# Performance work log

Measured on AMD Instinct MI355X. Metric: run time of the kernel, lower is better.

The kernel has to match this reference:

```python
import jax, jax.numpy as jnp
import numpy as np

DIM = 768
H = 12          # num_heads
KV = 4          # kv_heads
D = DIM // H    # head_dim = 64
ROPE_BASE = 10000.0
WINDOW = 8
B, N = 4, 1024


def setup_inputs() -> dict:
    key = jax.random.key(0)
    ks = jax.random.split(key, 8)
    s = 0.02  # weight scale for sane magnitudes
    return {
        "x": jax.random.normal(ks[0], (B, N, DIM), jnp.float32),
        "Wq": jax.random.normal(ks[1], (2 * DIM, DIM), jnp.float32) * s,
        "Wk": jax.random.normal(ks[2], (2 * DIM * KV // H, DIM), jnp.float32) * s,
        "Wv1": jax.random.normal(ks[3], (DIM * KV // H, DIM), jnp.float32) * s,
        "Wv2": jax.random.normal(ks[4], (DIM * KV // H, DIM), jnp.float32) * s,
        "lambda_p": jnp.full((H, 1, 1), -2.0, jnp.float32),
        "Wo": jax.random.normal(ks[5], (DIM, DIM), jnp.float32) * s,
        "bo": jax.random.normal(ks[6], (DIM,), jnp.float32) * s,
    }


def _rotate_half(x):
    x1 = x[..., ::2]
    x2 = x[..., 1::2]
    return jnp.stack([-x2, x1], axis=-1).reshape(x.shape)


def _rope_cos_sin(n, dtype):
    side = int(n ** 0.5)
    if side * side == n:
        h = np.arange(side, dtype=np.float32)
        gh, gw = np.meshgrid(h, h, indexing="ij")
        pos_h, pos_w = gh.reshape(-1), gw.reshape(-1)
    else:
        pos_h = np.arange(n, dtype=np.float32)
        pos_w = np.zeros_like(pos_h)
    dim_half = D // 2
    inv_freq = ROPE_BASE ** (-np.arange(dim_half, dtype=np.float32) / dim_half)
    theta = np.concatenate([pos_h[:, None] * inv_freq[None, :],
                            pos_w[:, None] * inv_freq[None, :]], axis=1)  # [N, D]
    cos = jnp.asarray(np.cos(theta), dtype)[None, None]  # [1,1,N,D]
    sin = jnp.asarray(np.sin(theta), dtype)[None, None]
    return cos, sin


def _apply_rope(q, cos, sin):
    return q * cos + _rotate_half(q) * sin


def _qk_norm(t):
    return t / (jnp.linalg.norm(t, axis=-1, keepdims=True) + 1e-6)


def _window_mask(n, dtype):
    side = int(n ** 0.5)
    if side * side == n:
        h = np.arange(side)
        gh, gw = np.meshgrid(h, h, indexing="ij")
        coords = np.stack([gh.reshape(-1), gw.reshape(-1)], axis=1)  # [N,2]
        dist = np.abs(coords[:, None, :] - coords[None, :, :]).max(-1)  # Chebyshev
    else:
        idx = np.arange(n)
        dist = np.abs(idx[None, :] - idx[:, None])
    return jnp.asarray(np.where(dist > WINDOW, -np.inf, 0.0).astype(np.float32), dtype)


def _attend(q, k, v, mask):
    # q,k,v: [B,H,N,D]; mask additive [N,N]
    scale = 1.0 / np.sqrt(D)
    scores = jnp.einsum("bhnd,bhmd->bhnm", q, k) * scale + mask
    return jnp.einsum("bhnm,bhmd->bhnd", jax.nn.softmax(scores, axis=-1), v)


def reference(x, Wq, Wk, Wv1, Wv2, lambda_p, Wo, bo):
    b, n, c = x.shape
    rep = H // KV
    q = (x @ Wq.T).reshape(b, n, 2, H, D).transpose(2, 0, 3, 1, 4)   # [2,B,H,N,D]
    k = (x @ Wk.T).reshape(b, n, 2, KV, D).transpose(2, 0, 3, 1, 4)  # [2,B,KV,N,D]
    v1 = (x @ Wv1.T).reshape(b, n, KV, D).transpose(0, 2, 1, 3)      # [B,KV,N,D]
    v2 = (x @ Wv2.T).reshape(b, n, KV, D).transpose(0, 2, 1, 3)
    q1, q2 = q[0], q[1]
    k1, k2 = k[0], k[1]
    # GQA: repeat_interleave over head axis
    k1 = jnp.repeat(k1, rep, axis=1)
    k2 = jnp.repeat(k2, rep, axis=1)
    v1 = jnp.repeat(v1, rep, axis=1)
    v2 = jnp.repeat(v2, rep, axis=1)
    cos, sin = _rope_cos_sin(n, x.dtype)
    q1, q2 = _apply_rope(q1, cos, sin), _apply_rope(q2, cos, sin)
    k1, k2 = _apply_rope(k1, cos, sin), _apply_rope(k2, cos, sin)
    q1, q2, k1, k2 = _qk_norm(q1), _qk_norm(q2), _qk_norm(k1), _qk_norm(k2)
    mask = _window_mask(n, x.dtype)
    out1 = _attend(q1, k1, v1, mask)
    out2 = _attend(q2, k2, v2, mask)
    lam = jax.nn.softplus(lambda_p)  # [H,1,1] broadcasts over [B,H,N,D]
    out = out1 - lam[None] * out2
    out = out.transpose(0, 2, 1, 3).reshape(b, n, c)
    return out @ Wo.T + bo
```

## Files before the change

kernel.cpp:

```cpp
#include <hip/hip_runtime.h>
#include <hip/hip_bf16.h>

#define BATCH 4
#define NSEQ  1024
#define DIM   768
#define NH    12
#define NKV   4
#define HD    64
#define NTOK  (BATCH*NSEQ)

using bf16 = __hip_bfloat16;
typedef __attribute__((ext_vector_type(8))) short short8;
typedef __attribute__((ext_vector_type(4))) float floatx4;

__device__ __forceinline__ float b2f(short x) {
  unsigned u = ((unsigned)(unsigned short)x) << 16;
  return __builtin_bit_cast(float, u);
}
__device__ __forceinline__ unsigned short f2b(float f) {
  unsigned u = __builtin_bit_cast(unsigned, f);
  unsigned r = u + 0x7FFF + ((u >> 16) & 1);
  return (unsigned short)(r >> 16);
}
__device__ __forceinline__ unsigned cvtpk(float lo, float hi) {
  unsigned r;
  asm("v_cvt_pk_bf16_f32 %0, %1, %2" : "=v"(r) : "v"(lo), "v"(hi));
  return r;
}

__device__ __forceinline__ void load_lds_16(const bf16* g, bf16* l) {
  __builtin_amdgcn_global_load_lds(
      (const __attribute__((address_space(1))) void*)g,
      (__attribute__((address_space(3))) void*)l, 16, 0, 0);
}

__global__ __launch_bounds__(256) void cvt_all(
    const float* __restrict__ x,  const float* __restrict__ wq,
    const float* __restrict__ wk, const float* __restrict__ wv1,
    const float* __restrict__ wv2, const float* __restrict__ wo,
    bf16* __restrict__ xb,  bf16* __restrict__ wqb, bf16* __restrict__ wkb,
    bf16* __restrict__ wv1b, bf16* __restrict__ wv2b, bf16* __restrict__ wob)
{
  int i = blockIdx.x * 256 + threadIdx.x;
  const float* s; bf16* d; int off;
  if      (i <  786432) { s = x;   d = xb;   off = i; }
  else if (i < 1081344) { s = wq;  d = wqb;  off = i -  786432; }
  else if (i < 1179648) { s = wk;  d = wkb;  off = i - 1081344; }
  else if (i < 1228800) { s = wv1; d = wv1b; off = i - 1179648; }
  else if (i < 1277952) { s = wv2; d = wv2b; off = i - 1228800; }
  else                  { s = wo;  d = wob;  off = i - 1277952; }
  float4 f = reinterpret_cast<const float4*>(s)[off];
  ushort4 u;
  u.x = f2b(f.x); u.y = f2b(f.y); u.z = f2b(f.z); u.w = f2b(f.w);
  reinterpret_cast<ushort4*>(d)[off] = u;
}

__global__ __launch_bounds__(256, 2) void gemm_qkv(
    const bf16* __restrict__ xb,
    const bf16* __restrict__ Wqb, const bf16* __restrict__ Wkb,
    const bf16* __restrict__ Wv1b, const bf16* __restrict__ Wv2b,
    bf16* __restrict__ Qpk, bf16* __restrict__ Kpk,
    bf16* __restrict__ Vpk1, bf16* __restrict__ Vpk2)
{
  __shared__ __align__(16) bf16 As[128 * 64];
  __shared__ __align__(16) bf16 Ws[128 * 64];

  const int bn = blockIdx.x, bm = blockIdx.y;
  const bf16* Wp;
  if (bn < 12)      Wp = Wqb  + (size_t)bn * 128 * 768;
  else if (bn < 16) Wp = Wkb  + (size_t)(bn - 12) * 128 * 768;
  else if (bn < 18) Wp = Wv1b + (size_t)(bn - 16) * 128 * 768;
  else              Wp = Wv2b + (size_t)(bn - 18) * 128 * 768;

  const int t = threadIdx.x, wave = t >> 6, lane = t & 63;
  const int wm = wave >> 1, wn = wave & 1;
  const int quad = lane >> 4, lr = lane & 15;

  const int srow = wave * 32 + (lane >> 3);
  const int scol = ((lane & 7) ^ (lane >> 3)) * 8;
  const bf16* Ag = xb + (size_t)(bm * 128 + srow) * 768 + scol;
  const bf16* Wg = Wp + (size_t)srow * 768 + scol;
  bf16* Al = As + wave * 32 * 64;
  bf16* Wl = Ws + wave * 32 * 64;

  floatx4 acc[4][4] = {};

  for (int k0 = 0; k0 < 768; k0 += 64) {
    #pragma unroll
    for (int c = 0; c < 4; ++c) {
      load_lds_16(Ag + (size_t)c * 8 * 768 + k0, Al + c * 8 * 64);
      load_lds_16(Wg + (size_t)c * 8 * 768 + k0, Wl + c * 8 * 64);
    }
    __syncthreads();

    short8 af[4][2], wf[4][2];
    #pragma unroll
    for (int mt = 0; mt < 4; ++mt)
      #pragma unroll
      for (int ks = 0; ks < 2; ++ks)
        af[mt][ks] = *reinterpret_cast<const short8*>(
            &As[(wm * 64 + mt * 16 + lr) * 64 + ((ks * 32 + quad * 8) ^ ((lr & 7) * 8))]);
    #pragma unroll
    for (int nt = 0; nt < 4; ++nt)
      #pragma unroll
      for (int ks = 0; ks < 2; ++ks)
        wf[nt][ks] = *reinterpret_cast<const short8*>(
            &Ws[(wn * 64 + nt * 16 + lr) * 64 + ((ks * 32 + quad * 8) ^ ((lr & 7) * 8))]);

    #pragma unroll
    for (int mt = 0; mt < 4; ++mt)
      #pragma unroll
      for (int nt = 0; nt < 4; ++nt) {
        acc[mt][nt] = __builtin_amdgcn_mfma_f32_16x16x32_bf16(af[mt][0], wf[nt][0], acc[mt][nt], 0, 0, 0);
        acc[mt][nt] = __builtin_amdgcn_mfma_f32_16x16x32_bf16(af[mt][1], wf[nt][1], acc[mt][nt], 0, 0, 0);
      }
    __syncthreads();
  }

  if (bn < 16) {
    const float K2 = 0.41524101186098309f;
    const float invf0 = exp2f(-(float)lr * K2);
    const float invf1 = exp2f(-(float)(16 + lr) * K2);
    const float sgn = (lr & 1) ? 1.f : -1.f;
    const bool isq = (bn < 12);
    const int hq = bn * 2 + wn;
    const int sq_ = hq / 12, hq_ = hq % 12;
    const int hh = (bn - 12) * 2 + wn;
    const int sk_ = hh >> 2, kvh_ = hh & 3;
    const int qk128 = (lr >> 3) * 128;
    #pragma unroll
    for (int mt = 0; mt < 4; ++mt) {
      const int row0 = bm * 128 + wm * 64 + mt * 16 + quad * 4;
      const int n0 = row0 & (NSEQ - 1);
      const int bb = row0 >> 10, kh = n0 >> 5;
      const float ph = (float)kh;
      const float pw0 = (float)(n0 & 31);
      const float t0 = ph * invf0, t1 = ph * invf1;
      const float c0 = __cosf(t0), s0 = __sinf(t0);
      const float c1 = __cosf(t1), s1 = __sinf(t1);
      bf16* tb0;
      if (isq) {
        tb0 = Qpk + ((size_t)((bb * 2 + sq_) * 12 + hq_) * 32 + kh) * 2048
              + (size_t)(mt & 1) * 1024 + qk128 + (quad * 4) * 8 + (lr & 7);
      } else {
        tb0 = Kpk + ((size_t)((bb * 2 + sk_) * 4 + kvh_) * 32 + kh) * 2048
              + (size_t)(mt & 1) * 1024 + qk128 + (quad * 4) * 8 + (lr & 7);
      }
      #pragma unroll
      for (int r = 0; r < 4; ++r) {
        float v0 = acc[mt][0][r];
        float v1 = acc[mt][1][r];
        float v2 = acc[mt][2][r];
        float v3 = acc[mt][3][r];
        float rot0 = sgn * __shfl_xor(v0, 1);
        float rot1 = sgn * __shfl_xor(v1, 1);
        float rot2 = sgn * __shfl_xor(v2, 1);
        float rot3 = sgn * __shfl_xor(v3, 1);
        float pw = pw0 + (float)r;
        float t2 = pw * invf0, t3 = pw * invf1;
        float rv0 = v0 * c0 + rot0 * s0;
        float rv1 = v1 * c1 + rot1 * s1;
        float rv2 = v2 * __cosf(t2) + rot2 * __sinf(t2);
        float rv3 = v3 * __cosf(t3) + rot3 * __sinf(t3);
        float ss = rv0 * rv0 + rv1 * rv1 + rv2 * rv2 + rv3 * rv3;
        #pragma unroll
        for (int off = 1; off < 16; off <<= 1) ss += __shfl_xor(ss, off);
        float sc = 1.f / (sqrtf(ss) + 1e-6f);
        if (isq) sc *= 0.18033688011112042f;
        bf16* tb = tb0 + r * 8;
        unsigned pkA = cvtpk(rv0 * sc, rv1 * sc);
        unsigned pkB = cvtpk(rv2 * sc, rv3 * sc);
        *(unsigned short*)&tb[0]   = (unsigned short)pkA;
        *(unsigned short*)&tb[256] = (unsigned short)(pkA >> 16);
        *(unsigned short*)&tb[512] = (unsigned short)pkB;
        *(unsigned short*)&tb[768] = (unsigned short)(pkB >> 16);
      }
    }
  } else {
    const bool is2 = (bn >= 18);
    bf16* Vp = is2 ? Vpk2 : Vpk1;
    const int kvh_ = (bn - (is2 ? 18 : 16)) * 2 + wn;
    #pragma unroll
    for (int mt = 0; mt < 4; ++mt)
      #pragma unroll
      for (int r = 0; r < 4; ++r) {
        int row = bm * 128 + wm * 64 + mt * 16 + quad * 4 + r;
        int n = row & (NSEQ - 1);
        int bb = row >> 10, kh = n >> 5;
        int rowm = (mt & 1) * 16 + quad * 4 + r;
        int quad_v = rowm >> 3, j = rowm & 7;
        bf16* tb = Vp + ((size_t)(bb * 4 + kvh_) * 32 + kh) * 2048
                   + quad_v * 128 + lr * 8 + j;
        unsigned pkA = cvtpk(acc[mt][0][r], acc[mt][1][r]);
        unsigned pkB = cvtpk(acc[mt][2][r], acc[mt][3][r]);
        *(unsigned short*)&tb[0]    = (unsigned short)pkA;
        *(unsigned short*)&tb[512]  = (unsigned short)(pkA >> 16);
        *(unsigned short*)&tb[1024] = (unsigned short)pkB;
        *(unsigned short*)&tb[1536] = (unsigned short)(pkB >> 16);
      }
  }
}

__global__ __launch_bounds__(256) void gemm_out(
    const bf16* __restrict__ Xb, const bf16* __restrict__ Wob,
    float* __restrict__ out, const float* __restrict__ bias)
{
  __shared__ __align__(16) bf16 As[64 * 64];
  __shared__ __align__(16) bf16 Ws[64 * 64];

  const int bn = blockIdx.x, bm = blockIdx.y;
  const int t = threadIdx.x, wave = t >> 6, lane = t & 63;
  const int wm = wave >> 1, wn = wave & 1;
  const int quad = lane >> 4, lr = lane & 15;

  const int srow = wave * 16 + (lane >> 3);
  const int scol = ((lane & 7) ^ (lane >> 3)) * 8;
  const bf16* Ag = Xb  + (size_t)(bm * 64 + srow) * 768 + scol;
  const bf16* Wg = Wob + (size_t)(bn * 64 + srow) * 768 + scol;
  bf16* Al = As + wave * 16 * 64;
  bf16* Wl = Ws + wave * 16 * 64;

  floatx4 acc[2][2] = {};

  for (int k0 = 0; k0 < 768; k0 += 64) {
    #pragma unroll
    for (int c = 0; c < 2; ++c) {
      load_lds_16(Ag + (size_t)c * 8 * 768 + k0, Al + c * 8 * 64);
      load_lds_16(Wg + (size_t)c * 8 * 768 + k0, Wl + c * 8 * 64);
    }
    __syncthreads();

    short8 af[2][2], wf[2][2];
    #pragma unroll
    for (int mt = 0; mt < 2; ++mt)
      #pragma unroll
      for (int ks = 0; ks < 2; ++ks)
        af[mt][ks] = *reinterpret_cast<const short8*>(
            &As[(wm * 32 + mt * 16 + lr) * 64 + ((ks * 32 + quad * 8) ^ ((lr & 7) * 8))]);
    #pragma unroll
    for (int nt = 0; nt < 2; ++nt)
      #pragma unroll
      for (int ks = 0; ks < 2; ++ks)
        wf[nt][ks] = *reinterpret_cast<const short8*>(
            &Ws[(wn * 32 + nt * 16 + lr) * 64 + ((ks * 32 + quad * 8) ^ ((lr & 7) * 8))]);

    #pragma unroll
    for (int mt = 0; mt < 2; ++mt)
      #pragma unroll
      for (int nt = 0; nt < 2; ++nt) {
        acc[mt][nt] = __builtin_amdgcn_mfma_f32_16x16x32_bf16(af[mt][0], wf[nt][0], acc[mt][nt], 0, 0, 0);
        acc[mt][nt] = __builtin_amdgcn_mfma_f32_16x16x32_bf16(af[mt][1], wf[nt][1], acc[mt][nt], 0, 0, 0);
      }
    __syncthreads();
  }

  #pragma unroll
  for (int nt = 0; nt < 2; ++nt) {
    int col = bn * 64 + wn * 32 + nt * 16 + lr;
    float bv = bias[col];
    #pragma unroll
    for (int mt = 0; mt < 2; ++mt)
      #pragma unroll
      for (int r = 0; r < 4; ++r) {
        int row = bm * 64 + wm * 32 + mt * 16 + quad * 4 + r;
        out[(size_t)row * 768 + col] = acc[mt][nt][r] + bv;
      }
  }
}

struct Frag { short8 kf[2][2]; short8 vf[4]; };

__device__ __forceinline__ void attn_load(
    Frag& f, const bf16* __restrict__ kp, const bf16* __restrict__ vp,
    int kh, int lane8)
{
  const bf16* kt = kp + (size_t)kh * 2048 + lane8;
  const bf16* vt = vp + (size_t)kh * 2048 + lane8;
  f.kf[0][0] = *reinterpret_cast<const short8*>(kt);
  f.kf[0][1] = *reinterpret_cast<const short8*>(kt + 512);
  f.kf[1][0] = *reinterpret_cast<const short8*>(kt + 1024);
  f.kf[1][1] = *reinterpret_cast<const short8*>(kt + 1536);
  f.vf[0] = *reinterpret_cast<const short8*>(vt);
  f.vf[1] = *reinterpret_cast<const short8*>(vt + 512);
  f.vf[2] = *reinterpret_cast<const short8*>(vt + 1024);
  f.vf[3] = *reinterpret_cast<const short8*>(vt + 1536);
}

__device__ __forceinline__ void attn_step(
    const short8 (&qf)[2][2], const Frag& f, unsigned maskbits,
    floatx4 (&O)[2][4], float (&psum)[2][4], bf16* __restrict__ Pl,
    int quad, int lr)
{
  floatx4 S[2][2] = {};
  #pragma unroll
  for (int ks = 0; ks < 2; ++ks) {
    S[0][0] = __builtin_amdgcn_mfma_f32_16x16x32_bf16(qf[0][ks], f.kf[0][ks], S[0][0], 0, 0, 0);
    S[0][1] = __builtin_amdgcn_mfma_f32_16x16x32_bf16(qf[0][ks], f.kf[1][ks], S[0][1], 0, 0, 0);
    S[1][0] = __builtin_amdgcn_mfma_f32_16x16x32_bf16(qf[1][ks], f.kf[0][ks], S[1][0], 0, 0, 0);
    S[1][1] = __builtin_amdgcn_mfma_f32_16x16x32_bf16(qf[1][ks], f.kf[1][ks], S[1][1], 0, 0, 0);
  }

  #pragma unroll
  for (int mt = 0; mt < 2; ++mt)
    #pragma unroll
    for (int nt = 0; nt < 2; ++nt) {
      float pr[4];
      #pragma unroll
      for (int r = 0; r < 4; ++r) {
        float p = __builtin_amdgcn_exp2f(S[mt][nt][r]);
        p = ((maskbits >> (mt * 8 + nt * 4 + r)) & 1u) ? p : 0.0f;
        psum[mt][r] += p;
        pr[r] = p;
      }
      unsigned pkA = cvtpk(pr[0], pr[1]);
      unsigned pkB = cvtpk(pr[2], pr[3]);
      unsigned short* bp = (unsigned short*)&Pl[(mt * 16 + quad * 4) * 40 + nt * 16 + lr];
      bp[0]   = (unsigned short)pkA;
      bp[40]  = (unsigned short)(pkA >> 16);
      bp[80]  = (unsigned short)pkB;
      bp[120] = (unsigned short)(pkB >> 16);
    }

  short8 pf0 = *reinterpret_cast<const short8*>(&Pl[(lr) * 40 + quad * 8]);
  short8 pf1 = *reinterpret_cast<const short8*>(&Pl[(16 + lr) * 40 + quad * 8]);
  #pragma unroll
  for (int ntd = 0; ntd < 4; ++ntd) {
    O[0][ntd] = __builtin_amdgcn_mfma_f32_16x16x32_bf16(pf0, f.vf[ntd], O[0][ntd], 0, 0, 0);
    O[1][ntd] = __builtin_amdgcn_mfma_f32_16x16x32_bf16(pf1, f.vf[ntd], O[1][ntd], 0, 0, 0);
  }
}

__global__ __launch_bounds__(256, 2) void attn_mfma(
    const bf16* __restrict__ Qpk, const bf16* __restrict__ Kpk,
    const bf16* __restrict__ Vpk1, const bf16* __restrict__ Vpk2,
    const float* __restrict__ lambda_p, bf16* __restrict__ X)
{
  __shared__ __align__(16) char smem[20480];

  const int bid = blockIdx.x;
  const int qh = bid & 31;
  const int hb = bid >> 5;
  const int h  = hb % 12;
  const int b  = hb / 12;
  const int kvh = h / 3;

  const int t = threadIdx.x;
  const int w = t >> 6;
  const int s = w >> 1;
  const int half = w & 1;
  const int lane = t & 63;
  const int quad = lane >> 4, lr = lane & 15;
  const int lane8 = lane * 8;

  bf16* Pl = (bf16*)(smem + w * 2560);
  float* myO = (float*)(smem + (s ? 10240 : 0));
  float* myP = (float*)(smem + (s ? 10240 : 0) + 8192);
  bf16* Xs = (bf16*)smem;

  const int tok0 = b * NSEQ + qh * 32;

  short8 qf[2][2];
  {
    const bf16* qt = Qpk + ((size_t)((b * 2 + s) * 12 + h) * 32 + qh) * 2048 + lane8;
    qf[0][0] = *reinterpret_cast<const short8*>(qt);
    qf[0][1] = *reinterpret_cast<const short8*>(qt + 512);
    qf[1][0] = *reinterpret_cast<const short8*>(qt + 1024);
    qf[1][1] = *reinterpret_cast<const short8*>(qt + 1536);
  }

  unsigned maskbits = 0;
  #pragma unroll
  for (int mt = 0; mt < 2; ++mt)
    #pragma unroll
    for (int nt = 0; nt < 2; ++nt)
      #pragma unroll
      for (int r = 0; r < 4; ++r) {
        int qq = mt * 16 + quad * 4 + r;
        int km = nt * 16 + lr;
        int d = km - qq; if (d < 0) d = -d;
        if (d <= 8) maskbits |= 1u << (mt * 8 + nt * 4 + r);
      }

  floatx4 O[2][4] = {};
  float psum[2][4] = {};

  const int kh0 = (qh > 8) ? qh - 8 : 0;
  const int kh1 = (qh < 23) ? qh + 8 : 31;
  const int cnt = kh1 - kh0 + 1;
  const int cA = (cnt + 1) >> 1;
  const int khA = half ? kh0 + cA : kh0;
  const int khB = half ? kh1 : kh0 + cA - 1;

  const bf16* kpbase = Kpk + (size_t)((b * 2 + s) * 4 + kvh) * 32 * 2048;
  const bf16* vpbase = (s ? Vpk2 : Vpk1) + (size_t)(b * 4 + kvh) * 32 * 2048;

  Frag fA, fB;
  attn_load(fA, kpbase, vpbase, khA, lane8);
  attn_load(fB, kpbase, vpbase, (khA + 1 <= khB) ? khA + 1 : khB, lane8);

  int i = khA;
  while (true) {
    attn_step(qf, fA, maskbits, O, psum, Pl, quad, lr);
    if (i == khB) break;
    ++i;
    attn_load(fA, kpbase, vpbase, (i + 1 <= khB) ? i + 1 : i, lane8);
    attn_step(qf, fB, maskbits, O, psum, Pl, quad, lr);
    if (i == khB) break;
    ++i;
    attn_load(fB, kpbase, vpbase, (i + 1 <= khB) ? i + 1 : i, lane8);
  }

  auto writeslab = [&]() {
    #pragma unroll
    for (int mt = 0; mt < 2; ++mt)
      #pragma unroll
      for (int ntd = 0; ntd < 4; ++ntd)
        *reinterpret_cast<floatx4*>(&myO[(mt * 4 + ntd) * 256 + lane * 4]) = O[mt][ntd];
    floatx4 p0, p1;
    p0[0] = psum[0][0]; p0[1] = psum[0][1]; p0[2] = psum[0][2]; p0[3] = psum[0][3];
    p1[0] = psum[1][0]; p1[1] = psum[1][1]; p1[2] = psum[1][2]; p1[3] = psum[1][3];
    *reinterpret_cast<floatx4*>(&myP[lane * 4])       = p0;
    *reinterpret_cast<floatx4*>(&myP[256 + lane * 4]) = p1;
  };
  auto readadd_norm = [&]() {
    #pragma unroll
    for (int mt = 0; mt < 2; ++mt)
      #pragma unroll
      for (int ntd = 0; ntd < 4; ++ntd)
        O[mt][ntd] += *reinterpret_cast<const floatx4*>(&myO[(mt * 4 + ntd) * 256 + lane * 4]);
    floatx4 p0 = *reinterpret_cast<const floatx4*>(&myP[lane * 4]);
    floatx4 p1 = *reinterpret_cast<const floatx4*>(&myP[256 + lane * 4]);
    #pragma unroll
    for (int r = 0; r < 4; ++r) { psum[0][r] += p0[r]; psum[1][r] += p1[r]; }
    #pragma unroll
    for (int off = 1; off < 16; off <<= 1)
      #pragma unroll
      for (int mt = 0; mt < 2; ++mt)
        #pragma unroll
        for (int r = 0; r < 4; ++r)
          psum[mt][r] += __shfl_xor(psum[mt][r], off);
    #pragma unroll
    for (int mt = 0; mt < 2; ++mt)
      #pragma unroll
      for (int r = 0; r < 4; ++r)
        psum[mt][r] = 1.f / psum[mt][r];
    #pragma unroll
    for (int mt = 0; mt < 2; ++mt)
      #pragma unroll
      for (int ntd = 0; ntd < 4; ++ntd)
        #pragma unroll
        for (int r = 0; r < 4; ++r)
          O[mt][ntd][r] *= psum[mt][r];
  };

  __syncthreads();
  if (half) writeslab();
  __syncthreads();
  if (!half) {
    readadd_norm();
    if (s) {
      #pragma unroll
      for (int mt = 0; mt < 2; ++mt)
        #pragma unroll
        for (int ntd = 0; ntd < 4; ++ntd)
          *reinterpret_cast<floatx4*>(&myO[(mt * 4 + ntd) * 256 + lane * 4]) = O[mt][ntd];
    }
  }
  __syncthreads();
  if (w == 0) {
    const float* O2s = (const float*)(smem + 10240);
    float lam = log1pf(__expf(lambda_p[h]));
    #pragma unroll
    for (int mt = 0; mt < 2; ++mt)
      #pragma unroll
      for (int ntd = 0; ntd < 4; ++ntd) {
        floatx4 o2 = *reinterpret_cast<const floatx4*>(&O2s[(mt * 4 + ntd) * 256 + lane * 4]);
        #pragma unroll
        for (int r = 0; r < 4; ++r) {
          float xv = O[mt][ntd][r] - lam * o2[r];
          *(unsigned short*)&Xs[(mt * 16 + quad * 4 + r) * 72 + ntd * 16 + lr] = f2b(xv);
        }
      }
  }
  __syncthreads();

  {
    int row = t >> 3, seg = t & 7;
    short8 xv = *reinterpret_cast<const short8*>(&Xs[row * 72 + seg * 8]);
    *reinterpret_cast<short8*>(X + (size_t)(tok0 + row) * 768 + h * 64 + seg * 8) = xv;
  }
}

extern "C" void kernel_launch(void* const* d_in, const int* in_sizes, int n_in,
                              void* d_out, int out_size, void* d_ws, size_t ws_size,
                              hipStream_t stream)
{
  const float* x        = (const float*)d_in[0];
  const float* Wq       = (const float*)d_in[1];
  const float* Wk       = (const float*)d_in[2];
  const float* Wv1      = (const float*)d_in[3];
  const float* Wv2      = (const float*)d_in[4];
  const float* lambda_p = (const float*)d_in[5];
  const float* Wo       = (const float*)d_in[6];
  const float* bo       = (const float*)d_in[7];
  float* out = (float*)d_out;

  bf16* xb   = (bf16*)d_ws;
  bf16* Wqb  = xb   + (size_t)NTOK * 768;
  bf16* Wkb  = Wqb  + (size_t)1536 * 768;
  bf16* Wv1b = Wkb  + (size_t)512 * 768;
  bf16* Wv2b = Wv1b + (size_t)256 * 768;
  bf16* Wob  = Wv2b + (size_t)256 * 768;
  bf16* Qpk  = Wob  + (size_t)768 * 768;
  bf16* Xb   = Qpk  + (size_t)NTOK * 1536;
  bf16* Vpk1 = Xb   + (size_t)NTOK * 768;
  bf16* Vpk2 = Vpk1 + (size_t)512 * 2048;
  bf16* Kpk  = Vpk2 + (size_t)512 * 2048;

  cvt_all<<<5568, 256, 0, stream>>>(x, Wq, Wk, Wv1, Wv2, Wo,
                                    xb, Wqb, Wkb, Wv1b, Wv2b, Wob);

  gemm_qkv<<<dim3(20, 32), 256, 0, stream>>>(xb, Wqb, Wkb, Wv1b, Wv2b,
                                             Qpk, Kpk, Vpk1, Vpk2);

  attn_mfma<<<BATCH * NH * 32, 256, 0, stream>>>(Qpk, Kpk, Vpk1, Vpk2, lambda_p, Xb);

  gemm_out<<<dim3(12, 64), 256, 0, stream>>>(Xb, Wob, out, bo);
}
```

Baseline: 146.5 us.

## Compute transposed scores and build P fragments via permlane swaps instead of LDS

Computes S transposed (K as the A operand) so each lane holds probabilities for a single query column. The P operand for the PV MFMA is then assembled in registers with v_permlane32_swap and shuffles, removing the per-step LDS round trip for P. Row sums become one scalar per query with a cheaper reduction, and the normalisation broadcasts the inverse through shuffles. The intent is to cut LDS traffic and waits in the inner loop, at the cost of extra cross-lane operations.

```diff
diff --git a/kernel.cpp b/kernel.cpp
--- a/kernel.cpp
+++ b/kernel.cpp
@@ -12,6 +12,7 @@
 using bf16 = __hip_bfloat16;
 typedef __attribute__((ext_vector_type(8))) short short8;
 typedef __attribute__((ext_vector_type(4))) float floatx4;
+typedef __attribute__((ext_vector_type(4))) unsigned uint4v;
 
 __device__ __forceinline__ float b2f(short x) {
   unsigned u = ((unsigned)(unsigned short)x) << 16;
@@ -288,45 +289,51 @@
 
 __device__ __forceinline__ void attn_step(
     const short8 (&qf)[2][2], const Frag& f, unsigned maskbits,
-    floatx4 (&O)[2][4], float (&psum)[2][4], bf16* __restrict__ Pl,
-    int quad, int lr)
-{
-  floatx4 S[2][2] = {};
+    floatx4 (&O)[2][4], float (&psum)[2], int quad)
+{
+  floatx4 St[2][2] = {};
   #pragma unroll
   for (int ks = 0; ks < 2; ++ks) {
-    S[0][0] = __builtin_amdgcn_mfma_f32_16x16x32_bf16(qf[0][ks], f.kf[0][ks], S[0][0], 0, 0, 0);
-    S[0][1] = __builtin_amdgcn_mfma_f32_16x16x32_bf16(qf[0][ks], f.kf[1][ks], S[0][1], 0, 0, 0);
-    S[1][0] = __builtin_amdgcn_mfma_f32_16x16x32_bf16(qf[1][ks], f.kf[0][ks], S[1][0], 0, 0, 0);
-    S[1][1] = __builtin_amdgcn_mfma_f32_16x16x32_bf16(qf[1][ks], f.kf[1][ks], S[1][1], 0, 0, 0);
-  }
-
+    St[0][0] = __builtin_amdgcn_mfma_f32_16x16x32_bf16(f.kf[0][ks], qf[0][ks], St[0][0], 0, 0, 0);
+    St[0][1] = __builtin_amdgcn_mfma_f32_16x16x32_bf16(f.kf[0][ks], qf[1][ks], St[0][1], 0, 0, 0);
+    St[1][0] = __builtin_amdgcn_mfma_f32_16x16x32_bf16(f.kf[1][ks], qf[0][ks], St[1][0], 0, 0, 0);
+    St[1][1] = __builtin_amdgcn_mfma_f32_16x16x32_bf16(f.kf[1][ks], qf[1][ks], St[1][1], 0, 0, 0);
+  }
+
+  unsigned pk[2][2][2];
   #pragma unroll
-  for (int mt = 0; mt < 2; ++mt)
-    #pragma unroll
-    for (int nt = 0; nt < 2; ++nt) {
+  for (int kt = 0; kt < 2; ++kt)
+    #pragma unroll
+    for (int mt = 0; mt < 2; ++mt) {
       float pr[4];
       #pragma unroll
       for (int r = 0; r < 4; ++r) {
-        float p = __builtin_amdgcn_exp2f(S[mt][nt][r]);
-        p = ((maskbits >> (mt * 8 + nt * 4 + r)) & 1u) ? p : 0.0f;
-        psum[mt][r] += p;
+        float p = __builtin_amdgcn_exp2f(St[kt][mt][r]);
+        p = ((maskbits >> (kt * 8 + mt * 4 + r)) & 1u) ? p : 0.0f;
+        psum[mt] += p;
         pr[r] = p;
       }
-      unsigned pkA = cvtpk(pr[0], pr[1]);
-      unsigned pkB = cvtpk(pr[2], pr[3]);
-      unsigned short* bp = (unsigned short*)&Pl[(mt * 16 + quad * 4) * 40 + nt * 16 + lr];
-      bp[0]   = (unsigned short)pkA;
-      bp[40]  = (unsigned short)(pkA >> 16);
-      bp[80]  = (unsigned short)pkB;
-      bp[120] = (unsigned short)(pkB >> 16);
-    }
-
-  short8 pf0 = *reinterpret_cast<const short8*>(&Pl[(lr) * 40 + quad * 8]);
-  short8 pf1 = *reinterpret_cast<const short8*>(&Pl[(16 + lr) * 40 + quad * 8]);
+      pk[kt][mt][0] = cvtpk(pr[0], pr[1]);
+      pk[kt][mt][1] = cvtpk(pr[2], pr[3]);
+    }
+
+  const bool oddq = (quad & 1);
   #pragma unroll
-  for (int ntd = 0; ntd < 4; ++ntd) {
-    O[0][ntd] = __builtin_amdgcn_mfma_f32_16x16x32_bf16(pf0, f.vf[ntd], O[0][ntd], 0, 0, 0);
-    O[1][ntd] = __builtin_amdgcn_mfma_f32_16x16x32_bf16(pf1, f.vf[ntd], O[1][ntd], 0, 0, 0);
+  for (int mt = 0; mt < 2; ++mt) {
+    uint4v regs;
+    #pragma unroll
+    for (int h = 0; h < 2; ++h) {
+      unsigned a = pk[0][mt][h], b = pk[1][mt][h];
+      asm("v_permlane32_swap_b32 %0, %1" : "+v"(a), "+v"(b));
+      unsigned sa = (unsigned)__shfl_xor((int)a, 16);
+      unsigned sb = (unsigned)__shfl_xor((int)b, 16);
+      regs[0 + h] = oddq ? sb : a;
+      regs[2 + h] = oddq ? b  : sa;
+    }
+    short8 pa = __builtin_bit_cast(short8, regs);
+    #pragma unroll
+    for (int ntd = 0; ntd < 4; ++ntd)
+      O[mt][ntd] = __builtin_amdgcn_mfma_f32_16x16x32_bf16(pa, f.vf[ntd], O[mt][ntd], 0, 0, 0);
   }
 }
 
@@ -352,7 +359,6 @@
   const int quad = lane >> 4, lr = lane & 15;
   const int lane8 = lane * 8;
 
-  bf16* Pl = (bf16*)(smem + w * 2560);
   float* myO = (float*)(smem + (s ? 10240 : 0));
   float* myP = (float*)(smem + (s ? 10240 : 0) + 8192);
   bf16* Xs = (bf16*)smem;
@@ -370,19 +376,19 @@
 
   unsigned maskbits = 0;
   #pragma unroll
-  for (int mt = 0; mt < 2; ++mt)
-    #pragma unroll
-    for (int nt = 0; nt < 2; ++nt)
+  for (int kt = 0; kt < 2; ++kt)
+    #pragma unroll
+    for (int mt = 0; mt < 2; ++mt)
       #pragma unroll
       for (int r = 0; r < 4; ++r) {
-        int qq = mt * 16 + quad * 4 + r;
-        int km = nt * 16 + lr;
-        int d = km - qq; if (d < 0) d = -d;
-        if (d <= 8) maskbits |= 1u << (mt * 8 + nt * 4 + r);
+        int wk = kt * 16 + quad * 4 + r;
+        int wq = mt * 16 + lr;
+        int d = wk - wq; if (d < 0) d = -d;
+        if (d <= 8) maskbits |= 1u << (kt * 8 + mt * 4 + r);
       }
 
   floatx4 O[2][4] = {};
-  float psum[2][4] = {};
+  float psum[2] = {};
 
   const int kh0 = (qh > 8) ? qh - 8 : 0;
   const int kh1 = (qh < 23) ? qh + 8 : 31;
@@ -400,11 +406,11 @@
 
   int i = khA;
   while (true) {
-    attn_step(qf, fA, maskbits, O, psum, Pl, quad, lr);
+    attn_step(qf, fA, maskbits, O, psum, quad);
     if (i == khB) break;
     ++i;
     attn_load(fA, kpbase, vpbase, (i + 1 <= khB) ? i + 1 : i, lane8);
-    attn_step(qf, fB, maskbits, O, psum, Pl, quad, lr);
+    attn_step(qf, fB, maskbits, O, psum, quad);
     if (i == khB) break;
     ++i;
     attn_load(fB, kpbase, vpbase, (i + 1 <= khB) ? i + 1 : i, lane8);
@@ -416,11 +422,8 @@
       #pragma unroll
       for (int ntd = 0; ntd < 4; ++ntd)
         *reinterpret_cast<floatx4*>(&myO[(mt * 4 + ntd) * 256 + lane * 4]) = O[mt][ntd];
-    floatx4 p0, p1;
-    p0[0] = psum[0][0]; p0[1] = psum[0][1]; p0[2] = psum[0][2]; p0[3] = psum[0][3];
-    p1[0] = psum[1][0]; p1[1] = psum[1][1]; p1[2] = psum[1][2]; p1[3] = psum[1][3];
-    *reinterpret_cast<floatx4*>(&myP[lane * 4])       = p0;
-    *reinterpret_cast<floatx4*>(&myP[256 + lane * 4]) = p1;
+    myP[lane]      = psum[0];
+    myP[64 + lane] = psum[1];
   };
   auto readadd_norm = [&]() {
     #pragma unroll
@@ -428,29 +431,26 @@
       #pragma unroll
       for (int ntd = 0; ntd < 4; ++ntd)
         O[mt][ntd] += *reinterpret_cast<const floatx4*>(&myO[(mt * 4 + ntd) * 256 + lane * 4]);
-    floatx4 p0 = *reinterpret_cast<const floatx4*>(&myP[lane * 4]);
-    floatx4 p1 = *reinterpret_cast<const floatx4*>(&myP[256 + lane * 4]);
-    #pragma unroll
-    for (int r = 0; r < 4; ++r) { psum[0][r] += p0[r]; psum[1][r] += p1[r]; }
-    #pragma unroll
-    for (int off = 1; off < 16; off <<= 1)
-      #pragma unroll
-      for (int mt = 0; mt < 2; ++mt)
-        #pragma unroll
-        for (int r = 0; r < 4; ++r)
-          psum[mt][r] += __shfl_xor(psum[mt][r], off);
-    #pragma unroll
-    for (int mt = 0; mt < 2; ++mt)
+    psum[0] += myP[lane];
+    psum[1] += myP[64 + lane];
+    #pragma unroll
+    for (int mt = 0; mt < 2; ++mt) {
+      psum[mt] += __shfl_xor(psum[mt], 16);
+      psum[mt] += __shfl_xor(psum[mt], 32);
+      psum[mt] = 1.f / psum[mt];
+    }
+    #pragma unroll
+    for (int mt = 0; mt < 2; ++mt) {
+      float invq[4];
       #pragma unroll
       for (int r = 0; r < 4; ++r)
-        psum[mt][r] = 1.f / psum[mt][r];
-    #pragma unroll
-    for (int mt = 0; mt < 2; ++mt)
+        invq[r] = __shfl(psum[mt], (lane & 48) + quad * 4 + r);
       #pragma unroll
       for (int ntd = 0; ntd < 4; ++ntd)
         #pragma unroll
         for (int r = 0; r < 4; ++r)
-          O[mt][ntd][r] *= psum[mt][r];
+          O[mt][ntd][r] *= invq[r];
+    }
   };
 
   __syncthreads();
```

Result: no change. 143.9 us (-1.8%).
